# Optimization experiments

Measured on AMD Instinct MI355X. Metric: run time of the kernel, lower is better.

The kernel has to match this reference:

```python
import math
import jax, jax.numpy as jnp
import numpy as np

B, L, C, H = 4, 2048, 1024, 16
D = C // H


def setup_inputs() -> dict:
    key = jax.random.key(0)
    k1, k2, k3 = jax.random.split(key, 3)
    x = jax.random.normal(k1, (B, L, C), dtype=jnp.float32)
    Wqkv = jax.random.normal(k2, (C, 3 * C), dtype=jnp.float32) * (1.0 / math.sqrt(C))
    bqkv = jax.random.normal(k3, (3 * C,), dtype=jnp.float32) * 0.02
    return {"x": x, "Wqkv": Wqkv, "bqkv": bqkv}


def reference(x, Wqkv, bqkv):
    b, l, c = x.shape
    h, d = H, c // H
    qkv = x @ Wqkv + bqkv                      # [B, L, 3C]
    q, k, v = jnp.split(qkv, 3, axis=-1)
    # [B, L, C] -> [B, H, L, D]
    q = q.reshape(b, l, h, d).transpose(0, 2, 1, 3)
    k = k.reshape(b, l, h, d).transpose(0, 2, 1, 3)
    v = v.reshape(b, l, h, d).transpose(0, 2, 1, 3)
    scale = 1.0 / math.sqrt(d)
    scores = jnp.einsum('bhld,bhmd->bhlm', q, k) * scale  # [B, H, L, L]
    causal = jnp.tril(jnp.ones((l, l), dtype=bool))       # [L, L]
    scores = jnp.where(causal[None, None, :, :], scores, -jnp.inf)
    attn = jax.nn.softmax(scores, axis=-1)
    y = jnp.einsum('bhlm,bhmd->bhld', attn, v)            # [B, H, L, D]
    y = y.transpose(0, 2, 1, 3).reshape(b, l, c)          # [B, L, C]
    return y
```

## Files before the change

### kernel.cpp

```cpp
#include <hip/hip_runtime.h>

#define L_SEQ 2048
#define CDIM  1024
#define NH    16
#define HD    64
#define NBH   64
#define KDIM  1024

typedef __attribute__((ext_vector_type(4))) float f32x4;
typedef __attribute__((ext_vector_type(8))) short s16x8;
typedef __attribute__((ext_vector_type(4))) short s16x4;

__device__ inline short f2bf(float f) {
  union { float f; unsigned u; } v; v.f = f;
  unsigned r = v.u + 0x7fffu + ((v.u >> 16) & 1u);
  return (short)(r >> 16);
}

__device__ inline f32x4 mfma16(s16x8 a, s16x8 b, f32x4 c) {
  return __builtin_amdgcn_mfma_f32_16x16x32_bf16(a, b, c, 0, 0, 0);
}

__device__ inline unsigned cvt_pk_bf16(float lo, float hi) {
  unsigned r;
  asm("v_cvt_pk_bf16_f32 %0, %1, %2" : "=v"(r) : "v"(lo), "v"(hi));
  return r;
}

__global__ __launch_bounds__(256) void convert_f32_bf16(const float* __restrict__ in,
                                                        short* __restrict__ out) {
  int i = (blockIdx.x * 256 + threadIdx.x) * 4;
  typedef __attribute__((ext_vector_type(4))) float fv4;
  fv4 v = *(const fv4*)(in + i);
  s16x4 o;
  o[0] = f2bf(v[0]); o[1] = f2bf(v[1]); o[2] = f2bf(v[2]); o[3] = f2bf(v[3]);
  *(s16x4*)(out + i) = o;
}

__global__ __launch_bounds__(256) void transpose_w(const float* __restrict__ W,
                                                   short* __restrict__ Wt) {
  __shared__ float tile[64][65];
  int n0 = blockIdx.x * 64, k0 = blockIdx.y * 64;
  int tc = threadIdx.x & 63, tr = threadIdx.x >> 6;
#pragma unroll
  for (int i = 0; i < 16; ++i) {
    int r = i * 4 + tr;
    tile[r][tc] = W[(size_t)(k0 + r) * 3072 + n0 + tc];
  }
  __syncthreads();
#pragma unroll
  for (int i = 0; i < 16; ++i) {
    int r = i * 4 + tr;
    Wt[(size_t)(n0 + r) * 1024 + k0 + tc] = f2bf(tile[tc][r]);
  }
}

__global__ __launch_bounds__(256) void transpose_v(const short* __restrict__ V,
                                                   short* __restrict__ Vt) {
  __shared__ short tile[64][72];
  int bh = blockIdx.y, l0 = blockIdx.x * 64;
  const short* Vb = V + (size_t)bh * L_SEQ * HD;
  short* Vtb = Vt + (size_t)bh * HD * L_SEQ;
  int tc = threadIdx.x & 63, tr = threadIdx.x >> 6;
#pragma unroll
  for (int i = 0; i < 16; ++i) {
    int r = i * 4 + tr;
    tile[r][tc] = Vb[(size_t)(l0 + r) * HD + tc];
  }
  __syncthreads();
#pragma unroll
  for (int i = 0; i < 16; ++i) {
    int r = i * 4 + tr;
    Vtb[(size_t)r * L_SEQ + l0 + tc] = tile[tc][r];
  }
}

#define BKP 40
__global__ __launch_bounds__(256) void qkv_gemm(const short* __restrict__ A,
                                                const short* __restrict__ Bt,
                                                const float* __restrict__ bias,
                                                short* __restrict__ Qo,
                                                short* __restrict__ Ko,
                                                short* __restrict__ Vo) {
  __shared__ __align__(16) short As[128 * BKP];
  __shared__ __align__(16) short Bs[128 * BKP];
  const int t = threadIdx.x;
  const int lane = t & 63, wid = t >> 6;
  const int wm = wid >> 1, wn = wid & 1;
  const int lrow = lane & 15, lg = lane >> 4;
  const int tm = blockIdx.x * 128, tn = blockIdx.y * 128;

  f32x4 acc[4][4];
#pragma unroll
  for (int i = 0; i < 4; ++i)
#pragma unroll
    for (int j = 0; j < 4; ++j) { acc[i][j][0]=0.f; acc[i][j][1]=0.f; acc[i][j][2]=0.f; acc[i][j][3]=0.f; }

  for (int kt = 0; kt < KDIM; kt += 32) {
    __syncthreads();
#pragma unroll
    for (int c = 0; c < 2; ++c) {
      int q = t + 256 * c;
      int row = q >> 2, koff = (q & 3) * 8;
      s16x8 av = *(const s16x8*)(A + (size_t)(tm + row) * KDIM + kt + koff);
      *(s16x8*)(As + row * BKP + koff) = av;
      s16x8 bv = *(const s16x8*)(Bt + (size_t)(tn + row) * KDIM + kt + koff);
      *(s16x8*)(Bs + row * BKP + koff) = bv;
    }
    __syncthreads();
    s16x8 af[4], bf[4];
#pragma unroll
    for (int i = 0; i < 4; ++i)
      af[i] = *(const s16x8*)(As + (wm * 64 + i * 16 + lrow) * BKP + lg * 8);
#pragma unroll
    for (int j = 0; j < 4; ++j)
      bf[j] = *(const s16x8*)(Bs + (wn * 64 + j * 16 + lrow) * BKP + lg * 8);
#pragma unroll
    for (int i = 0; i < 4; ++i)
#pragma unroll
      for (int j = 0; j < 4; ++j)
        acc[i][j] = mfma16(af[i], bf[j], acc[i][j]);
  }

  const float QS = 0.125f * 1.4426950408889634f;
#pragma unroll
  for (int i = 0; i < 4; ++i)
#pragma unroll
    for (int j = 0; j < 4; ++j) {
      int n = tn + wn * 64 + j * 16 + lrow;
      float bv = bias[n];
      int s = n >> 10, rem = n & 1023;
      int h = rem >> 6, d = rem & 63;
#pragma unroll
      for (int r = 0; r < 4; ++r) {
        int m = tm + wm * 64 + i * 16 + lg * 4 + r;
        int b = m >> 11, l = m & 2047;
        float v = acc[i][j][r] + bv;
        size_t idx = ((size_t)(b * NH + h) * L_SEQ + l) * HD + d;
        if (s == 0)      Qo[idx] = f2bf(v * QS);
        else if (s == 1) Ko[idx] = f2bf(v);
        else             Vo[idx] = f2bf(v);
      }
    }
}

__global__ __launch_bounds__(256) void attn(const short* __restrict__ Q,
                                            const short* __restrict__ K,
                                            const short* __restrict__ Vt,
                                            float* __restrict__ out) {
  const int t = threadIdx.x, lane = t & 63, wid = t >> 6;
  const int lrow = lane & 15, lg = lane >> 4;
  const int bh = blockIdx.y;
  const size_t bhoff = (size_t)bh * L_SEQ * HD;
  const short* Qb = Q + bhoff;
  const short* Kb = K + bhoff;
  const short* Vb = Vt + (size_t)bh * HD * L_SEQ;
  const int b = bh >> 4, h = bh & 15;
  const int src0 = lrow + ((lane & 16) << 1);
  const int src1 = src0 + 16;
  const bool hi_nf = (lg & 2) != 0;

#pragma unroll
  for (int tt = 0; tt < 2; ++tt) {
    const int qt = tt ? (31 - (int)blockIdx.x) : (int)blockIdx.x;
    const int q0 = qt * 64 + wid * 16;
    const int qi = q0 + lrow;

    s16x8 qf0 = *(const s16x8*)(Qb + (size_t)qi * HD + lg * 8);
    s16x8 qf1 = *(const s16x8*)(Qb + (size_t)qi * HD + 32 + lg * 8);

    f32x4 o[4];
#pragma unroll
    for (int dt = 0; dt < 4; ++dt) { o[dt][0]=0.f; o[dt][1]=0.f; o[dt][2]=0.f; o[dt][3]=0.f; }
    float mr = -1e30f, lr = 0.f;

    const int kvend = q0 + 16;
    for (int kv0 = 0; kv0 < kvend; kv0 += 64) {
      s16x8 vf[2][4];
#pragma unroll
      for (int ks = 0; ks < 2; ++ks)
#pragma unroll
        for (int dt = 0; dt < 4; ++dt)
          vf[ks][dt] = *(const s16x8*)(Vb + (size_t)(dt * 16 + lrow) * L_SEQ + kv0 + ks * 32 + lg * 8);

      f32x4 s[4];
#pragma unroll
      for (int nf = 0; nf < 4; ++nf) {
        f32x4 sv; sv[0]=0.f; sv[1]=0.f; sv[2]=0.f; sv[3]=0.f;
        const short* Krow = Kb + (size_t)(kv0 + nf * 16 + lrow) * HD;
        sv = mfma16(*(const s16x8*)(Krow + lg * 8), qf0, sv);
        sv = mfma16(*(const s16x8*)(Krow + 32 + lg * 8), qf1, sv);
        s[nf] = sv;
      }
      if (kv0 + 63 > q0) {
#pragma unroll
        for (int nf = 0; nf < 4; ++nf)
#pragma unroll
          for (int r = 0; r < 4; ++r)
            if (kv0 + nf * 16 + lg * 4 + r > qi) s[nf][r] = -INFINITY;
      }
      float mt = s[0][0];
#pragma unroll
      for (int nf = 0; nf < 4; ++nf)
#pragma unroll
        for (int r = 0; r < 4; ++r) mt = fmaxf(mt, s[nf][r]);
      mt = fmaxf(mt, __shfl_xor(mt, 16));
      mt = fmaxf(mt, __shfl_xor(mt, 32));
      float mn = fmaxf(mr, mt);
      float fr = exp2f(mr - mn);
      mr = mn;
      float ps = 0.f;
#pragma unroll
      for (int nf = 0; nf < 4; ++nf)
#pragma unroll
        for (int r = 0; r < 4; ++r) {
          float p = exp2f(s[nf][r] - mn);
          s[nf][r] = p; ps += p;
        }
      ps += __shfl_xor(ps, 16);
      ps += __shfl_xor(ps, 32);
      lr = lr * fr + ps;
#pragma unroll
      for (int dt = 0; dt < 4; ++dt) o[dt] *= fr;

      unsigned w0[4], w1[4];
#pragma unroll
      for (int nf = 0; nf < 4; ++nf) {
        w0[nf] = cvt_pk_bf16(s[nf][0], s[nf][1]);
        w1[nf] = cvt_pk_bf16(s[nf][2], s[nf][3]);
      }

#pragma unroll
      for (int ks = 0; ks < 2; ++ks) {
        int a0 = __shfl((int)w0[2 * ks],     src0);
        int a1 = __shfl((int)w0[2 * ks + 1], src0);
        int b0 = __shfl((int)w1[2 * ks],     src0);
        int b1 = __shfl((int)w1[2 * ks + 1], src0);
        int c0 = __shfl((int)w0[2 * ks],     src1);
        int c1 = __shfl((int)w0[2 * ks + 1], src1);
        int d0 = __shfl((int)w1[2 * ks],     src1);
        int d1 = __shfl((int)w1[2 * ks + 1], src1);
        union { int i[4]; s16x8 v; } pu;
        pu.i[0] = hi_nf ? a1 : a0;
        pu.i[1] = hi_nf ? b1 : b0;
        pu.i[2] = hi_nf ? c1 : c0;
        pu.i[3] = hi_nf ? d1 : d0;
#pragma unroll
        for (int dt = 0; dt < 4; ++dt)
          o[dt] = mfma16(vf[ks][dt], pu.v, o[dt]);
      }
    }

    const float inv = 1.0f / lr;
    const size_t obase = (size_t)(b * L_SEQ + qi) * CDIM + h * HD + lg * 4;
#pragma unroll
    for (int dt = 0; dt < 4; ++dt) {
      f32x4 ov = o[dt] * inv;
      *(f32x4*)(out + obase + dt * 16) = ov;
    }
  }
}

extern "C" void kernel_launch(void* const* d_in, const int* in_sizes, int n_in,
                              void* d_out, int out_size, void* d_ws, size_t ws_size,
                              hipStream_t stream) {
  const float* x    = (const float*)d_in[0];
  const float* W    = (const float*)d_in[1];
  const float* bqkv = (const float*)d_in[2];
  float* out = (float*)d_out;
  char* ws = (char*)d_ws;

  const size_t SZ_XB  = (size_t)8192 * 1024 * 2;
  const size_t SZ_WT  = (size_t)3072 * 1024 * 2;
  const size_t SZ_HEAD = (size_t)NBH * L_SEQ * HD * 2;

  short* xb  = (short*)ws;
  short* wtb = (short*)(ws + SZ_XB);
  short* Qo  = (short*)(ws + SZ_XB + SZ_WT);
  short* Ko  = (short*)(ws + SZ_XB + SZ_WT + SZ_HEAD);
  short* Vo  = (short*)(ws + SZ_XB + SZ_WT + 2 * SZ_HEAD);
  short* Vtb = (short*)ws;

  convert_f32_bf16<<<8192, 256, 0, stream>>>(x, xb);
  transpose_w<<<dim3(48, 16), 256, 0, stream>>>(W, wtb);
  qkv_gemm<<<dim3(64, 24), 256, 0, stream>>>(xb, wtb, bqkv, Qo, Ko, Vo);
  transpose_v<<<dim3(32, 64), 256, 0, stream>>>(Vo, Vtb);
  attn<<<dim3(16, 64), 256, 0, stream>>>(Qo, Ko, Vtb, out);
}
```

Before: 404.7 us.

## Use direct global-to-LDS loads with XOR swizzle and BK=64 in QKV GEMM

The QKV projection GEMM now stages A and B tiles with global_load_lds, which moves data straight into LDS instead of passing it through registers. The K step is doubled to 64, halving the number of barriers per tile. An XOR swizzle on the 16-byte chunks replaces the padded layout to avoid LDS bank conflicts. The loop stays single-buffered with a full vmcnt wait, so load latency is still not overlapped with MFMA work.

```diff
diff --git a/kernel.cpp b/kernel.cpp
--- a/kernel.cpp
+++ b/kernel.cpp
@@ -25,6 +25,12 @@
   unsigned r;
   asm("v_cvt_pk_bf16_f32 %0, %1, %2" : "=v"(r) : "v"(lo), "v"(hi));
   return r;
+}
+
+__device__ inline void gload_lds16(const short* g, short* l) {
+  __builtin_amdgcn_global_load_lds(
+      (const __attribute__((address_space(1))) unsigned*)g,
+      (__attribute__((address_space(3))) unsigned*)l, 16, 0, 0);
 }
 
 __global__ __launch_bounds__(256) void convert_f32_bf16(const float* __restrict__ in,
@@ -75,51 +81,62 @@
   }
 }
 
-#define BKP 40
 __global__ __launch_bounds__(256) void qkv_gemm(const short* __restrict__ A,
                                                 const short* __restrict__ Bt,
                                                 const float* __restrict__ bias,
                                                 short* __restrict__ Qo,
                                                 short* __restrict__ Ko,
                                                 short* __restrict__ Vo) {
-  __shared__ __align__(16) short As[128 * BKP];
-  __shared__ __align__(16) short Bs[128 * BKP];
+  __shared__ __align__(16) short As[128 * 64];
+  __shared__ __align__(16) short Bs[128 * 64];
   const int t = threadIdx.x;
   const int lane = t & 63, wid = t >> 6;
   const int wm = wid >> 1, wn = wid & 1;
   const int lrow = lane & 15, lg = lane >> 4;
   const int tm = blockIdx.x * 128, tn = blockIdx.y * 128;
 
+  const int srow = lane >> 3;
+  const int schunk = (lane & 7) ^ srow;
+  const int sw = lrow & 7;
+
   f32x4 acc[4][4];
 #pragma unroll
   for (int i = 0; i < 4; ++i)
 #pragma unroll
     for (int j = 0; j < 4; ++j) { acc[i][j][0]=0.f; acc[i][j][1]=0.f; acc[i][j][2]=0.f; acc[i][j][3]=0.f; }
 
-  for (int kt = 0; kt < KDIM; kt += 32) {
+  for (int kt = 0; kt < KDIM; kt += 64) {
     __syncthreads();
 #pragma unroll
-    for (int c = 0; c < 2; ++c) {
-      int q = t + 256 * c;
-      int row = q >> 2, koff = (q & 3) * 8;
-      s16x8 av = *(const s16x8*)(A + (size_t)(tm + row) * KDIM + kt + koff);
-      *(s16x8*)(As + row * BKP + koff) = av;
-      s16x8 bv = *(const s16x8*)(Bt + (size_t)(tn + row) * KDIM + kt + koff);
-      *(s16x8*)(Bs + row * BKP + koff) = bv;
-    }
+    for (int ii = 0; ii < 4; ++ii) {
+      int row0 = wid * 32 + ii * 8;
+      int rowg = row0 + srow;
+      gload_lds16(A  + (size_t)(tm + rowg) * KDIM + kt + schunk * 8, &As[row0 * 64]);
+      gload_lds16(Bt + (size_t)(tn + rowg) * KDIM + kt + schunk * 8, &Bs[row0 * 64]);
+    }
+    asm volatile("s_waitcnt vmcnt(0)" ::: "memory");
     __syncthreads();
-    s16x8 af[4], bf[4];
+
+    s16x8 af[4][2], bf[4][2];
+#pragma unroll
+    for (int i = 0; i < 4; ++i) {
+      int row = wm * 64 + i * 16 + lrow;
+      af[i][0] = *(const s16x8*)(As + row * 64 + ((lg)     ^ sw) * 8);
+      af[i][1] = *(const s16x8*)(As + row * 64 + ((4 + lg) ^ sw) * 8);
+    }
+#pragma unroll
+    for (int j = 0; j < 4; ++j) {
+      int row = wn * 64 + j * 16 + lrow;
+      bf[j][0] = *(const s16x8*)(Bs + row * 64 + ((lg)     ^ sw) * 8);
+      bf[j][1] = *(const s16x8*)(Bs + row * 64 + ((4 + lg) ^ sw) * 8);
+    }
 #pragma unroll
     for (int i = 0; i < 4; ++i)
-      af[i] = *(const s16x8*)(As + (wm * 64 + i * 16 + lrow) * BKP + lg * 8);
-#pragma unroll
-    for (int j = 0; j < 4; ++j)
-      bf[j] = *(const s16x8*)(Bs + (wn * 64 + j * 16 + lrow) * BKP + lg * 8);
-#pragma unroll
-    for (int i = 0; i < 4; ++i)
-#pragma unroll
-      for (int j = 0; j < 4; ++j)
-        acc[i][j] = mfma16(af[i], bf[j], acc[i][j]);
+#pragma unroll
+      for (int j = 0; j < 4; ++j) {
+        acc[i][j] = mfma16(af[i][0], bf[j][0], acc[i][j]);
+        acc[i][j] = mfma16(af[i][1], bf[j][1], acc[i][j]);
+      }
   }
 
   const float QS = 0.125f * 1.4426950408889634f;
```

Result: no change. 400.0 us (-1.2%).
